# Kernel optimization log

Hardware: AMD Instinct MI355X
Metric: run time of the kernel (lower is better)

Reference implementation:

```python
import jax, jax.numpy as jnp
import numpy as np

L = 8       # num decoder layers
S = 192     # seq_len = h*w = 24*8
D = 512     # d_model
DFF = 2048  # dim_feedforward
H, W, BS = 24, 8, 16
EPS = 1e-5


def setup_inputs() -> dict:
    key = jax.random.key(0)
    ks = jax.random.split(key, 8)
    f = jax.random.normal
    return {
        "q_feat": f(ks[0], (BS, D * L, H, W), jnp.float32),
        "g_feat": f(ks[1], (BS, D * L, H, W), jnp.float32),
        "targets": jax.random.randint(ks[2], (BS,), 0, 8),
        "score_embed": f(ks[3], (L, S, S), jnp.float32) * 0.05,
        "fc0_w": f(ks[4], (L, D, D), jnp.float32) * (1.0 / np.sqrt(D)),
        "fc0_b": jnp.zeros((L, D), jnp.float32),
        "bn1_g": jnp.ones((L,), jnp.float32),
        "bn1_b": jnp.zeros((L,), jnp.float32),
        "fc2_w": f(ks[5], (L, DFF, S), jnp.float32) * (1.0 / np.sqrt(S)),
        "fc2_b": jnp.zeros((L, DFF), jnp.float32),
        "bn2_g": jnp.ones((L, DFF), jnp.float32),
        "bn2_b": jnp.zeros((L, DFF), jnp.float32),
        "fc3_w": f(ks[6], (L, DFF), jnp.float32) * (1.0 / np.sqrt(DFF)),
        "fc3_b": jnp.zeros((L,), jnp.float32),
        "bn3_g": jnp.ones((L,), jnp.float32),
        "bn3_b": jnp.zeros((L,), jnp.float32),
    }


def _layer(qf, gf, se, w0, b0, g1, b1, w2, b2, g2, bb2, w3, b3, g3, bb3):
    # qf: [q,s,d], gf: [k,s,d]; shared fc0 projection for query and key
    query = jnp.einsum('qsd,ed->qse', qf, w0) + b0
    key_ = jnp.einsum('ksd,ed->kse', gf, w0) + b0
    # 4D correlation volume masked by sigmoid of learned score embedding
    score = jnp.einsum('qtd,ksd->qkst', query, key_) * jax.nn.sigmoid(se)
    q, k = score.shape[0], score.shape[1]
    sc = score.reshape(q * k, S, S)
    cat = jnp.concatenate([sc.max(axis=1), sc.max(axis=2)], axis=-1)  # [qk, 2S]
    x = cat.reshape(-1, S)  # [2qk, S]  (matches torch view(-1,1,S))
    # bn1: single channel -> normalize over all elements (training-mode BN)
    x = g1 * (x - x.mean()) * jax.lax.rsqrt(x.var() + EPS) + b1
    x = x @ w2.T + b2  # [2qk, DFF]
    mu = x.mean(0)
    var = x.var(0)
    x = g2 * (x - mu) * jax.lax.rsqrt(var + EPS) + bb2
    x = jax.nn.relu(x)
    x = x @ w3 + b3  # [2qk]
    x = x.reshape(-1, 2).sum(-1)  # [qk]: sum of row-max branch and col-max branch
    x = g3 * (x - x.mean()) * jax.lax.rsqrt(x.var() + EPS) + bb3
    return x.reshape(q, k)


def reference(q_feat, g_feat, targets, score_embed, fc0_w, fc0_b, bn1_g, bn1_b,
              fc2_w, fc2_b, bn2_g, bn2_b, fc3_w, fc3_b, bn3_g, bn3_b):
    bs = q_feat.shape[0]
    qf = jnp.transpose(q_feat, (0, 2, 3, 1)).reshape(bs, S, D * L)
    gf = jnp.transpose(g_feat, (0, 2, 3, 1)).reshape(bs, S, D * L)
    score = None
    for i in range(L):  # fixed small layer loop; each layer has distinct params
        si = _layer(qf[..., i * D:(i + 1) * D], gf[..., i * D:(i + 1) * D],
                    score_embed[i], fc0_w[i], fc0_b[i], bn1_g[i], bn1_b[i],
                    fc2_w[i], fc2_b[i], bn2_g[i], bn2_b[i],
                    fc3_w[i], fc3_b[i], bn3_g[i], bn3_b[i])
        score = si if score is None else score + si
    pair_labels = (targets[:, None] == targets[None, :]).astype(jnp.float32)
    return score, pair_labels
```

## Files before the change

### kernel.cpp

```cpp
#include <hip/hip_runtime.h>
#include <hip/hip_bf16.h>


#define EPS_ 1e-5f

typedef __attribute__((ext_vector_type(8))) _Float16 fp16x8;
typedef __attribute__((ext_vector_type(4)))  float   f32x4;
typedef __attribute__((ext_vector_type(16))) float   f32x16;

__device__ __forceinline__ unsigned fkey(float f) {
    unsigned u = __float_as_uint(f);
    return (u & 0x80000000u) ? ~u : (u | 0x80000000u);
}
__device__ __forceinline__ float funkey(unsigned k) {
    return (k & 0x80000000u) ? __uint_as_float(k & 0x7FFFFFFFu)
                             : __uint_as_float(~k);
}
__device__ __forceinline__ void gld16(const void* gp, void* lp) {
    __builtin_amdgcn_global_load_lds(
        (const __attribute__((address_space(1))) unsigned*)gp,
        (__attribute__((address_space(3))) unsigned*)lp, 16, 0, 0);
}

__global__ __launch_bounds__(256) void k_prep(const float* __restrict__ se,
                                              float* __restrict__ sig,
                                              const float* __restrict__ w2,
                                              _Float16* __restrict__ w2h,
                                              unsigned* __restrict__ xkey,
                                              float* __restrict__ bn2z) {
    int b = blockIdx.x;
    int tid = threadIdx.x;
    if (b < 3072) {
        int i = b * 256 + tid;
        float4 v = *(const float4*)(w2 + (size_t)i * 4);
        _Float16 h[4] = {(_Float16)v.x, (_Float16)v.y, (_Float16)v.z, (_Float16)v.w};
        *(uint2*)(w2h + (size_t)i * 4) = *(uint2*)h;
    } else if (b < 3360) {
        int i = (b - 3072) * 256 + tid;
        float4 v = *(const float4*)(se + (size_t)i * 4);
        float4 o;
        o.x = 1.f / (1.f + __expf(-v.x));
        o.y = 1.f / (1.f + __expf(-v.y));
        o.z = 1.f / (1.f + __expf(-v.z));
        o.w = 1.f / (1.f + __expf(-v.w));
        *(float4*)(sig + (size_t)i * 4) = o;
    } else if (b < 3552) {
        int i = (b - 3360) * 256 + tid;
        uint4 z = {0u, 0u, 0u, 0u};
        uint4* p = (uint4*)xkey + (size_t)i * 4;
        p[0] = z; p[1] = z; p[2] = z; p[3] = z;
    } else {
        int i = (b - 3552) * 256 + tid;
        if (i < 8196) {
            float4 z = {0.f, 0.f, 0.f, 0.f};
            *(float4*)(bn2z + (size_t)i * 4) = z;
        }
    }
}

__global__ __launch_bounds__(256) void k_fc0(const float* __restrict__ qfeat,
                                             const float* __restrict__ gfeat,
                                             const float* __restrict__ w0,
                                             const float* __restrict__ b0,
                                             _Float16* __restrict__ Qh) {
    int bid = blockIdx.x;
    int et = bid & 1;  bid >>= 1;
    int tt = bid % 3;  bid /= 3;
    int b  = bid & 15; bid >>= 4;
    int l  = bid & 7;  bid >>= 3;
    int sel = bid;
    const float* feat  = sel ? gfeat : qfeat;
    const float* Af = feat + (size_t)b * 4096 * 192 + (size_t)l * 512 * 192;
    const float* Wf = w0 + (size_t)l * 262144;
    int t0 = tt * 64, e0 = et * 256;

    __shared__ __align__(16) char At[64 * 80];
    __shared__ __align__(16) char Bt[256 * 80];

    int tid = threadIdx.x;
    int lane = tid & 63;
    int w = tid >> 6;
    int half = lane >> 5;
    int lrow = lane & 31;

    f32x16 acc[2][2];
    #pragma unroll
    for (int mi = 0; mi < 2; mi++)
        #pragma unroll
        for (int ni = 0; ni < 2; ni++)
            #pragma unroll
            for (int r = 0; r < 16; r++) acc[mi][ni][r] = 0.f;

    for (int d0 = 0; d0 < 512; d0 += 32) {
        __syncthreads();
        {
            int tA = tid & 63;
            int dp = tid >> 6;
            #pragma unroll
            for (int r = 0; r < 4; r++) {
                int d = dp * 2 + r * 8;
                float v0 = Af[(size_t)(d0 + d) * 192 + t0 + tA];
                float v1 = Af[(size_t)(d0 + d + 1) * 192 + t0 + tA];
                _Float16 h2[2] = {(_Float16)v0, (_Float16)v1};
                *(unsigned*)(At + tA * 80 + d * 2) = *(unsigned*)h2;
            }
        }
        {
            #pragma unroll
            for (int p = 0; p < 8; p++) {
                int s = tid + p * 256;
                int e = s >> 3;
                int q = s & 7;
                float4 wv = *(const float4*)(Wf + (size_t)(e0 + e) * 512 + d0 + q * 4);
                _Float16 h[4] = {(_Float16)wv.x, (_Float16)wv.y, (_Float16)wv.z, (_Float16)wv.w};
                *(uint2*)(Bt + e * 80 + q * 8) = *(uint2*)h;
            }
        }
        __syncthreads();
        #pragma unroll
        for (int ks = 0; ks < 2; ks++) {
            int koff = ks * 32 + half * 16;
            fp16x8 a[2], bf[2];
            #pragma unroll
            for (int mi = 0; mi < 2; mi++)
                a[mi] = *(const fp16x8*)(At + (mi * 32 + lrow) * 80 + koff);
            #pragma unroll
            for (int ni = 0; ni < 2; ni++)
                bf[ni] = *(const fp16x8*)(Bt + (w * 64 + ni * 32 + lrow) * 80 + koff);
            #pragma unroll
            for (int mi = 0; mi < 2; mi++)
                #pragma unroll
                for (int ni = 0; ni < 2; ni++)
                    acc[mi][ni] = __builtin_amdgcn_mfma_f32_32x32x16_f16(a[mi], bf[ni], acc[mi][ni], 0, 0, 0);
        }
    }

    _Float16* Obase = Qh + ((size_t)(sel * 8 + l) * 16 + b) * 98304;
    #pragma unroll
    for (int ni = 0; ni < 2; ni++) {
        int e = e0 + w * 64 + ni * 32 + lrow;
        float bias = b0[l * 512 + e];
        #pragma unroll
        for (int mi = 0; mi < 2; mi++) {
            #pragma unroll
            for (int r = 0; r < 16; r++) {
                int t = t0 + mi * 32 + (r & 3) + 8 * (r >> 2) + 4 * half;
                Obase[(size_t)t * 512 + e] = (_Float16)(acc[mi][ni][r] + bias);
            }
        }
    }
}

#define BARP() do { __builtin_amdgcn_s_barrier(); \
                    __builtin_amdgcn_sched_barrier(0); } while (0)

__global__ __launch_bounds__(512, 2) void k_score(const _Float16* __restrict__ Qh,
                                                  const float* __restrict__ sig,
                                                  unsigned* __restrict__ xkey) {
    int bid = blockIdx.x;
    int l = bid & 7;
    int tau = bid >> 3;
    int mt = tau % 12;
    int nt = tau / 12;
    int m0 = mt * 256, n0 = nt * 256;

    const char* Ag = (const char*)(Qh + (size_t)(8 + l) * 1572864);
    const char* Bg = (const char*)(Qh + (size_t)l * 1572864);

    __shared__ __align__(16) char smem[131072];

    int tid = threadIdx.x;
    int lane = tid & 63;
    int w = tid >> 6;
    int wm = w >> 2, wn = w & 3;
    int c = lane & 15;
    int hi4 = lane >> 4;

    int pk0 = ((hi4)     ^ (c & 7)) * 16;
    int pk1 = ((4 + hi4) ^ (c & 7)) * 16;
    char* aBase = smem + wm * 16384 + c * 128;
    char* bBase = smem + 65536 + (wn >> 1) * 16384 + ((wn & 1) * 64 + c) * 128;

    int rl = lane >> 3;
    int qsw = ((lane & 7) ^ rl) * 16;
    const char* Asrc = Ag + (size_t)(m0 + w * 8 + rl) * 1024 + qsw;
    const char* Bsrc = Bg + (size_t)(n0 + w * 8 + rl) * 1024 + qsw;
    char* aSt = smem + w * 1024;
    char* bSt = smem + 65536 + w * 1024;

    f32x4 acc[8][4];
    #pragma unroll
    for (int mi = 0; mi < 8; mi++)
        #pragma unroll
        for (int nj = 0; nj < 4; nj++)
            #pragma unroll
            for (int r = 0; r < 4; r++) acc[mi][nj][r] = 0.f;

    fp16x8 a[4][2], b01[2][2], b23[2][2];

    auto STA = [&](int t, int h) {
        if (t < 8) {
            const char* s = Asrc + (size_t)(h * 128) * 1024 + t * 128;
            char* d = aSt + (t & 1) * 32768 + h * 16384;
            gld16(s, d);
            gld16(s + 64 * 1024, d + 8192);
        }
    };
    auto STB = [&](int t, int h) {
        if (t < 8) {
            const char* s = Bsrc + (size_t)(h * 128) * 1024 + t * 128;
            char* d = bSt + (t & 1) * 32768 + h * 16384;
            gld16(s, d);
            gld16(s + 64 * 1024, d + 8192);
        }
    };
    auto LDA = [&](int t, int mh) {
        const char* p = aBase + (t & 1) * 32768 + mh * 8192;
        #pragma unroll
        for (int m = 0; m < 4; m++) {
            a[m][0] = *(const fp16x8*)(p + m * 2048 + pk0);
            a[m][1] = *(const fp16x8*)(p + m * 2048 + pk1);
        }
    };
    auto LDB = [&](int t, int nh, fp16x8 (&bb)[2][2]) {
        const char* p = bBase + (t & 1) * 32768 + nh * 4096;
        #pragma unroll
        for (int n = 0; n < 2; n++) {
            bb[n][0] = *(const fp16x8*)(p + n * 2048 + pk0);
            bb[n][1] = *(const fp16x8*)(p + n * 2048 + pk1);
        }
    };
    auto MM = [&](int mh, int nh, fp16x8 (&bb)[2][2]) {
        #pragma unroll
        for (int ks = 0; ks < 2; ks++)
            #pragma unroll
            for (int m = 0; m < 4; m++)
                #pragma unroll
                for (int n = 0; n < 2; n++)
                    acc[mh * 4 + m][nh * 2 + n] = __builtin_amdgcn_mfma_f32_16x16x32_f16(
                        a[m][ks], bb[n][ks], acc[mh * 4 + m][nh * 2 + n], 0, 0, 0);
    };

    STB(0, 0); STB(0, 1); STA(0, 0); STA(0, 1); STB(1, 0); STB(1, 1);
    asm volatile("s_waitcnt vmcnt(4)");
    BARP();

    #pragma unroll
    for (int it = 0; it < 4; it++) {
        int T = 2 * it, U = 2 * it + 1;
        LDA(T, 0); LDB(T, 0, b01); STA(U, 0); BARP();
        __builtin_amdgcn_s_setprio(1); MM(0, 0, b01); __builtin_amdgcn_s_setprio(0); BARP();
        LDB(T, 1, b23); STA(U, 1); BARP();
        __builtin_amdgcn_s_setprio(1); MM(0, 1, b23); __builtin_amdgcn_s_setprio(0); BARP();
        LDA(T, 1); STB(T + 2, 0); BARP();
        __builtin_amdgcn_s_setprio(1); MM(1, 0, b01); __builtin_amdgcn_s_setprio(0); BARP();
        STB(T + 2, 1); BARP();
        __builtin_amdgcn_s_setprio(1); MM(1, 1, b23); __builtin_amdgcn_s_setprio(0);
        if (it < 3) { asm volatile("s_waitcnt vmcnt(4)"); }
        else        { asm volatile("s_waitcnt vmcnt(0)"); }
        BARP();
        LDA(U, 0); LDB(U, 0, b01); STA(T + 2, 0); BARP();
        __builtin_amdgcn_s_setprio(1); MM(0, 0, b01); __builtin_amdgcn_s_setprio(0); BARP();
        LDB(U, 1, b23); STA(T + 2, 1); BARP();
        __builtin_amdgcn_s_setprio(1); MM(0, 1, b23); __builtin_amdgcn_s_setprio(0); BARP();
        LDA(U, 1); STB(T + 3, 0); BARP();
        __builtin_amdgcn_s_setprio(1); MM(1, 0, b01); __builtin_amdgcn_s_setprio(0); BARP();
        STB(T + 3, 1); BARP();
        __builtin_amdgcn_s_setprio(1); MM(1, 1, b23); __builtin_amdgcn_s_setprio(0);
        if (it < 3) { asm volatile("s_waitcnt vmcnt(4)"); }
        BARP();
    }

    __syncthreads();

    int rq = hi4 * 4;
    int gcb = n0 + wn * 64;
    int qq = gcb / 192;
    int tb = gcb - qq * 192;
    (void)qq;
    const float* sg = sig + (size_t)l * 36864;

    float rowm[8][4];
    float colm[2][4];
    #pragma unroll
    for (int mi = 0; mi < 8; mi++)
        #pragma unroll
        for (int r = 0; r < 4; r++) rowm[mi][r] = -3.4e38f;
    #pragma unroll
    for (int h = 0; h < 2; h++)
        #pragma unroll
        for (int nj = 0; nj < 4; nj++) colm[h][nj] = -3.4e38f;

    #pragma unroll
    for (int mi = 0; mi < 8; mi++) {
        int gm = m0 + wm * 128 + mi * 16;
        int sb = gm % 192;
        #pragma unroll
        for (int r = 0; r < 4; r++) {
            const float* sp = sg + (size_t)(sb + rq + r) * 192 + tb;
            #pragma unroll
            for (int nj = 0; nj < 4; nj++) {
                float v = acc[mi][nj][r] * sp[nj * 16 + c];
                rowm[mi][r] = fmaxf(rowm[mi][r], v);
                colm[mi >> 2][nj] = fmaxf(colm[mi >> 2][nj], v);
            }
        }
    }
    #pragma unroll
    for (int st = 1; st <= 8; st <<= 1)
        #pragma unroll
        for (int mi = 0; mi < 8; mi++)
            #pragma unroll
            for (int r = 0; r < 4; r++)
                rowm[mi][r] = fmaxf(rowm[mi][r], __shfl_xor(rowm[mi][r], st));
    #pragma unroll
    for (int h = 0; h < 2; h++)
        #pragma unroll
        for (int nj = 0; nj < 4; nj++) {
            colm[h][nj] = fmaxf(colm[h][nj], __shfl_xor(colm[h][nj], 16));
            colm[h][nj] = fmaxf(colm[h][nj], __shfl_xor(colm[h][nj], 32));
        }

    unsigned* red = (unsigned*)smem;
    if (c == 0) {
        #pragma unroll
        for (int mi = 0; mi < 8; mi++)
            #pragma unroll
            for (int r = 0; r < 4; r++)
                red[w * 256 + mi * 16 + rq + r] = fkey(rowm[mi][r]);
    }
    if (lane < 16) {
        #pragma unroll
        for (int h = 0; h < 2; h++)
            #pragma unroll
            for (int nj = 0; nj < 4; nj++)
                red[w * 256 + 128 + h * 64 + nj * 16 + lane] = fkey(colm[h][nj]);
    }
    __syncthreads();
    #pragma unroll
    for (int pass = 0; pass < 4; pass++) {
        int flat = pass * 512 + tid;
        unsigned val = red[flat];
        int ww = flat >> 8;
        int rem = flat & 255;
        int wmf = ww >> 2, wnf = ww & 3;
        int gcbf = n0 + wnf * 64;
        int qqf = gcbf / 192;
        size_t addr;
        if (rem < 128) {
            int gmf = m0 + wmf * 128 + rem;
            int kkf = gmf / 192;
            int sf = gmf - kkf * 192;
            addr = ((size_t)l * 512 + 2 * (qqf * 16 + kkf) + 1) * 192 + sf;
        } else {
            int ii = rem - 128;
            int hh = ii >> 6, cc = ii & 63;
            int kkf = (m0 + wmf * 128 + hh * 64) / 192;
            addr = ((size_t)l * 512 + 2 * (qqf * 16 + kkf)) * 192 + (gcbf - qqf * 192) + cc;
        }
        atomicMax(&xkey[addr], val);
    }
}

__global__ __launch_bounds__(256) void k_bn1s(const unsigned* __restrict__ xkey,
                                              float* __restrict__ bn1acc) {
    int l = blockIdx.x / 48;
    int b = blockIdx.x - l * 48;
    const unsigned* xk = xkey + (size_t)l * 98304 + b * 2048;
    int tid = threadIdx.x;
    uint4 v1 = *(const uint4*)(xk + tid * 8);
    uint4 v2 = *(const uint4*)(xk + tid * 8 + 4);
    float s = 0.f, s2 = 0.f;
    float e;
    e = funkey(v1.x); s += e; s2 += e * e;
    e = funkey(v1.y); s += e; s2 += e * e;
    e = funkey(v1.z); s += e; s2 += e * e;
    e = funkey(v1.w); s += e; s2 += e * e;
    e = funkey(v2.x); s += e; s2 += e * e;
    e = funkey(v2.y); s += e; s2 += e * e;
    e = funkey(v2.z); s += e; s2 += e * e;
    e = funkey(v2.w); s += e; s2 += e * e;
    #pragma unroll
    for (int o = 32; o; o >>= 1) { s += __shfl_down(s, o); s2 += __shfl_down(s2, o); }
    if ((tid & 63) == 0) {
        atomicAdd(&bn1acc[l * 2], s);
        atomicAdd(&bn1acc[l * 2 + 1], s2);
    }
}

__global__ __launch_bounds__(256) void k_bn1n(const unsigned* __restrict__ xkey,
                                              const float* __restrict__ bn1acc,
                                              const float* __restrict__ g1,
                                              const float* __restrict__ b1,
                                              _Float16* __restrict__ xh) {
    int idx = blockIdx.x * 256 + threadIdx.x;
    int l = idx / 24576;
    float mu = bn1acc[l * 2] * (1.f / 98304.f);
    float var = bn1acc[l * 2 + 1] * (1.f / 98304.f) - mu * mu;
    float a1 = g1[l] * rsqrtf(var + EPS_);
    float c1 = b1[l] - mu * a1;
    uint4 kv = *(const uint4*)(xkey + (size_t)idx * 4);
    _Float16 h[4];
    h[0] = (_Float16)(funkey(kv.x) * a1 + c1);
    h[1] = (_Float16)(funkey(kv.y) * a1 + c1);
    h[2] = (_Float16)(funkey(kv.z) * a1 + c1);
    h[3] = (_Float16)(funkey(kv.w) * a1 + c1);
    *(uint2*)(xh + (size_t)idx * 4) = *(uint2*)h;
}

__global__ __launch_bounds__(256) void k_fc2(const _Float16* __restrict__ xh,
                                             const _Float16* __restrict__ w2h,
                                             const float* __restrict__ b2,
                                             _Float16* __restrict__ hb,
                                             float* __restrict__ bn2sum,
                                             float* __restrict__ bn2sq) {
    int bid = blockIdx.x;
    int l = bid >> 6;
    int rem = bid & 63;
    int mt = rem & 3, nt = rem >> 2;
    int m0 = mt * 128, n0 = nt * 128;
    const char* Ag = (const char*)(xh + (size_t)l * 98304);
    const char* Bg = (const char*)(w2h + (size_t)l * 393216);

    __shared__ __align__(16) char As[8192];
    __shared__ __align__(16) char Bs[8192];

    int tid = threadIdx.x;
    int lane = tid & 63;
    int w = tid >> 6;
    int wm = w >> 1, wn = w & 1;

    f32x4 acc[4][4];
    #pragma unroll
    for (int mi = 0; mi < 4; mi++)
        #pragma unroll
        for (int nj = 0; nj < 4; nj++)
            #pragma unroll
            for (int r = 0; r < 4; r++) acc[mi][nj][r] = 0.f;

    int srow = lane >> 2;
    int sseg = ((lane & 3) ^ ((srow >> 1) & 3)) * 16;
    int c = lane & 15;
    int kqp = (((lane >> 4) ^ ((c >> 1) & 3))) * 16;

    for (int d0 = 0; d0 < 384; d0 += 64) {
        __syncthreads();
        #pragma unroll
        for (int j = 0; j < 2; j++) {
            int r = w * 32 + j * 16 + srow;
            gld16(Ag + (size_t)(m0 + r) * 384 + d0 + sseg, As + (w * 32 + j * 16) * 64);
            gld16(Bg + (size_t)(n0 + r) * 384 + d0 + sseg, Bs + (w * 32 + j * 16) * 64);
        }
        __syncthreads();
        fp16x8 a[4], b[4];
        #pragma unroll
        for (int mi = 0; mi < 4; mi++)
            a[mi] = *(const fp16x8*)(As + (wm * 64 + mi * 16 + c) * 64 + kqp);
        #pragma unroll
        for (int nj = 0; nj < 4; nj++)
            b[nj] = *(const fp16x8*)(Bs + (wn * 64 + nj * 16 + c) * 64 + kqp);
        #pragma unroll
        for (int mi = 0; mi < 4; mi++)
            #pragma unroll
            for (int nj = 0; nj < 4; nj++)
                acc[mi][nj] = __builtin_amdgcn_mfma_f32_16x16x32_f16(a[mi], b[nj], acc[mi][nj], 0, 0, 0);
    }

    int rq = (lane >> 4) * 4;
    _Float16* ho = hb + (size_t)l * 1048576;
    float colsum[4], colsq[4];
    #pragma unroll
    for (int nj = 0; nj < 4; nj++) { colsum[nj] = 0.f; colsq[nj] = 0.f; }
    #pragma unroll
    for (int nj = 0; nj < 4; nj++) {
        int gf = n0 + wn * 64 + nj * 16 + c;
        float bias = b2[l * 2048 + gf];
        #pragma unroll
        for (int mi = 0; mi < 4; mi++) {
            #pragma unroll
            for (int r = 0; r < 4; r++) {
                int gm = m0 + wm * 64 + mi * 16 + rq + r;
                float v = acc[mi][nj][r] + bias;
                ho[(size_t)gm * 2048 + gf] = (_Float16)v;
                colsum[nj] += v;
                colsq[nj] += v * v;
            }
        }
    }
    #pragma unroll
    for (int nj = 0; nj < 4; nj++) {
        colsum[nj] += __shfl_xor(colsum[nj], 16);
        colsum[nj] += __shfl_xor(colsum[nj], 32);
        colsq[nj]  += __shfl_xor(colsq[nj], 16);
        colsq[nj]  += __shfl_xor(colsq[nj], 32);
    }
    if (lane < 16) {
        #pragma unroll
        for (int nj = 0; nj < 4; nj++) {
            int gf = n0 + wn * 64 + nj * 16 + lane;
            atomicAdd(&bn2sum[l * 2048 + gf], colsum[nj]);
            atomicAdd(&bn2sq[l * 2048 + gf], colsq[nj]);
        }
    }
}

__global__ __launch_bounds__(256) void k_fc3(const _Float16* __restrict__ hb,
                                             const float* __restrict__ bn2sum,
                                             const float* __restrict__ bn2sq,
                                             const float* __restrict__ g2,
                                             const float* __restrict__ bb2,
                                             const float* __restrict__ w3,
                                             const float* __restrict__ b3,
                                             float* __restrict__ ybuf) {
    int n = blockIdx.x & 511;
    int l = blockIdx.x >> 9;
    const _Float16* h = hb + ((size_t)l * 512 + n) * 2048;
    int tid = threadIdx.x;
    int f0 = tid * 8;
    fp16x8 hv = *(const fp16x8*)(h + f0);
    float sum = 0.f;
    #pragma unroll
    for (int j = 0; j < 8; j++) {
        int f = f0 + j;
        float mu = bn2sum[l * 2048 + f] * (1.f / 512.f);
        float var = bn2sq[l * 2048 + f] * (1.f / 512.f) - mu * mu;
        float a2 = g2[l * 2048 + f] * rsqrtf(var + EPS_);
        float c2 = bb2[l * 2048 + f] - mu * a2;
        float v = (float)hv[j] * a2 + c2;
        v = fmaxf(v, 0.f);
        sum += v * w3[l * 2048 + f];
    }
    __shared__ float red[4];
    int lane = tid & 63, w = tid >> 6;
    #pragma unroll
    for (int o = 32; o; o >>= 1) sum += __shfl_down(sum, o);
    if (lane == 0) red[w] = sum;
    __syncthreads();
    if (tid == 0) ybuf[l * 512 + n] = red[0] + red[1] + red[2] + red[3] + b3[l];
}

__global__ __launch_bounds__(256) void k_final(const float* __restrict__ ybuf,
                                               const float* __restrict__ g3,
                                               const float* __restrict__ bb3,
                                               const int* __restrict__ targets,
                                               float* __restrict__ out) {
    int tid = threadIdx.x;
    __shared__ float red[8];
    float scoreacc = 0.f;
    for (int l = 0; l < 8; l++) {
        float z = ybuf[l * 512 + 2 * tid] + ybuf[l * 512 + 2 * tid + 1];
        float s = z, s2 = z * z;
        int lane = tid & 63, w = tid >> 6;
        #pragma unroll
        for (int o = 32; o; o >>= 1) { s += __shfl_down(s, o); s2 += __shfl_down(s2, o); }
        if (lane == 0) { red[w] = s; red[4 + w] = s2; }
        __syncthreads();
        float S1 = red[0] + red[1] + red[2] + red[3];
        float S2 = red[4] + red[5] + red[6] + red[7];
        float mu = S1 * (1.f / 256.f);
        float var = S2 * (1.f / 256.f) - mu * mu;
        float rstd = rsqrtf(var + EPS_);
        scoreacc += g3[l] * (z - mu) * rstd + bb3[l];
        __syncthreads();
    }
    out[tid] = scoreacc;
    int i = tid >> 4, j = tid & 15;
    out[256 + tid] = (targets[i] == targets[j]) ? 1.f : 0.f;
}

extern "C" void kernel_launch(void* const* d_in, const int* in_sizes, int n_in,
                              void* d_out, int out_size, void* d_ws, size_t ws_size,
                              hipStream_t stream) {
    const float* q_feat = (const float*)d_in[0];
    const float* g_feat = (const float*)d_in[1];
    const int*   targets = (const int*)d_in[2];
    const float* se     = (const float*)d_in[3];
    const float* fc0_w  = (const float*)d_in[4];
    const float* fc0_b  = (const float*)d_in[5];
    const float* bn1_g  = (const float*)d_in[6];
    const float* bn1_b  = (const float*)d_in[7];
    const float* fc2_w  = (const float*)d_in[8];
    const float* fc2_b  = (const float*)d_in[9];
    const float* bn2_g  = (const float*)d_in[10];
    const float* bn2_b  = (const float*)d_in[11];
    const float* fc3_w  = (const float*)d_in[12];
    const float* fc3_b  = (const float*)d_in[13];
    const float* bn3_g  = (const float*)d_in[14];
    const float* bn3_b  = (const float*)d_in[15];

    float* ws = (float*)d_ws;
    _Float16* Qh   = (_Float16*)ws;
    float*    sig  = ws + 12582912;
    unsigned* xkey = (unsigned*)(ws + 12877824);
    _Float16* xh   = (_Float16*)(ws + 13664256);
    _Float16* w2h  = (_Float16*)(ws + 14057472);
    _Float16* hb   = (_Float16*)(ws + 15630336);
    float* bn2sum = ws + 19824640;
    float* bn2sq  = ws + 19841024;
    float* bn1acc = ws + 19857408;
    float* ybuf   = ws + 19857424;
    float* out  = (float*)d_out;

    k_prep<<<3585, 256, 0, stream>>>(se, sig, fc2_w, w2h, xkey, bn2sum);
    k_fc0<<<1536, 256, 0, stream>>>(q_feat, g_feat, fc0_w, fc0_b, Qh);
    k_score<<<1152, 512, 0, stream>>>(Qh, sig, xkey);
    k_bn1s<<<384, 256, 0, stream>>>(xkey, bn1acc);
    k_bn1n<<<768, 256, 0, stream>>>(xkey, bn1acc, bn1_g, bn1_b, xh);
    k_fc2<<<512, 256, 0, stream>>>(xh, w2h, fc2_b, hb, bn2sum, bn2sq);
    k_fc3<<<4096, 256, 0, stream>>>(hb, bn2sum, bn2sq, bn2_g, bn2_b, fc3_w, fc3_b, ybuf);
    k_final<<<1, 256, 0, stream>>>(ybuf, bn3_g, bn3_b, targets, out);
}
```

Baseline: 406.8 us.

## Split score kernel into chunked launches and precompute BN2 coefficients

The single k_score launch is split into five launches over block-index ranges via a base offset, likely to change scheduling and wave quantization across the GPU's CUs. A new k_coef kernel computes the BN2 scale and shift once per feature, reusing the sig buffer as storage. k_fc3 then loads these coefficients as float4 vectors instead of recomputing mean, variance and rsqrt in each of its 4096 blocks. The extra launches add fixed overhead and serialize the score chunks, which can leave CUs idle at each chunk tail.

New measurement: 410.0 us. Within noise of the previous version (+0.8%).

```diff
diff --git a/kernel.cpp b/kernel.cpp
--- a/kernel.cpp
+++ b/kernel.cpp
@@ -156,8 +156,9 @@
 
 __global__ __launch_bounds__(512, 2) void k_score(const _Float16* __restrict__ Qh,
                                                   const float* __restrict__ sig,
-                                                  unsigned* __restrict__ xkey) {
-    int bid = blockIdx.x;
+                                                  unsigned* __restrict__ xkey,
+                                                  int base) {
+    int bid = blockIdx.x + base;
     int l = bid & 7;
     int tau = bid >> 3;
     int mt = tau % 12;
@@ -504,11 +505,21 @@
     }
 }
 
+__global__ __launch_bounds__(256) void k_coef(const float* __restrict__ bn2sum,
+                                              const float* __restrict__ bn2sq,
+                                              const float* __restrict__ g2,
+                                              const float* __restrict__ bb2,
+                                              float* __restrict__ coef) {
+    int i = blockIdx.x * 256 + threadIdx.x;
+    float mu = bn2sum[i] * (1.f / 512.f);
+    float var = bn2sq[i] * (1.f / 512.f) - mu * mu;
+    float a2 = g2[i] * rsqrtf(var + EPS_);
+    coef[i] = a2;
+    coef[16384 + i] = bb2[i] - mu * a2;
+}
+
 __global__ __launch_bounds__(256) void k_fc3(const _Float16* __restrict__ hb,
-                                             const float* __restrict__ bn2sum,
-                                             const float* __restrict__ bn2sq,
-                                             const float* __restrict__ g2,
-                                             const float* __restrict__ bb2,
+                                             const float* __restrict__ coef,
                                              const float* __restrict__ w3,
                                              const float* __restrict__ b3,
                                              float* __restrict__ ybuf) {
@@ -518,17 +529,21 @@
     int tid = threadIdx.x;
     int f0 = tid * 8;
     fp16x8 hv = *(const fp16x8*)(h + f0);
+    const float* cA = coef + l * 2048 + f0;
+    const float* cC = coef + 16384 + l * 2048 + f0;
+    const float* w3p = w3 + l * 2048 + f0;
+    float4 a0 = *(const float4*)(cA), a1 = *(const float4*)(cA + 4);
+    float4 c0 = *(const float4*)(cC), c1 = *(const float4*)(cC + 4);
+    float4 w0 = *(const float4*)(w3p), w1 = *(const float4*)(w3p + 4);
     float sum = 0.f;
+    float va[8] = {a0.x, a0.y, a0.z, a0.w, a1.x, a1.y, a1.z, a1.w};
+    float vc[8] = {c0.x, c0.y, c0.z, c0.w, c1.x, c1.y, c1.z, c1.w};
+    float vw[8] = {w0.x, w0.y, w0.z, w0.w, w1.x, w1.y, w1.z, w1.w};
     #pragma unroll
     for (int j = 0; j < 8; j++) {
-        int f = f0 + j;
-        float mu = bn2sum[l * 2048 + f] * (1.f / 512.f);
-        float var = bn2sq[l * 2048 + f] * (1.f / 512.f) - mu * mu;
-        float a2 = g2[l * 2048 + f] * rsqrtf(var + EPS_);
-        float c2 = bb2[l * 2048 + f] - mu * a2;
-        float v = (float)hv[j] * a2 + c2;
+        float v = (float)hv[j] * va[j] + vc[j];
         v = fmaxf(v, 0.f);
-        sum += v * w3[l * 2048 + f];
+        sum += v * vw[j];
     }
     __shared__ float red[4];
     int lane = tid & 63, w = tid >> 6;
@@ -603,10 +618,15 @@
 
     k_prep<<<3585, 256, 0, stream>>>(se, sig, fc2_w, w2h, xkey, bn2sum);
     k_fc0<<<1536, 256, 0, stream>>>(q_feat, g_feat, fc0_w, fc0_b, Qh);
-    k_score<<<1152, 512, 0, stream>>>(Qh, sig, xkey);
+    k_score<<<256, 512, 0, stream>>>(Qh, sig, xkey, 0);
+    k_score<<<256, 512, 0, stream>>>(Qh, sig, xkey, 256);
+    k_score<<<256, 512, 0, stream>>>(Qh, sig, xkey, 512);
+    k_score<<<256, 512, 0, stream>>>(Qh, sig, xkey, 768);
+    k_score<<<128, 512, 0, stream>>>(Qh, sig, xkey, 1024);
     k_bn1s<<<384, 256, 0, stream>>>(xkey, bn1acc);
     k_bn1n<<<768, 256, 0, stream>>>(xkey, bn1acc, bn1_g, bn1_b, xh);
     k_fc2<<<512, 256, 0, stream>>>(xh, w2h, fc2_b, hb, bn2sum, bn2sq);
-    k_fc3<<<4096, 256, 0, stream>>>(hb, bn2sum, bn2sq, bn2_g, bn2_b, fc3_w, fc3_b, ybuf);
+    k_coef<<<64, 256, 0, stream>>>(bn2sum, bn2sq, bn2_g, bn2_b, sig);
+    k_fc3<<<4096, 256, 0, stream>>>(hb, sig, fc3_w, fc3_b, ybuf);
     k_final<<<1, 256, 0, stream>>>(ybuf, bn3_g, bn3_b, targets, out);
 }
```
